# Kernel optimization log

Measured on AMD Instinct MI355X. Metric: run time of the kernel, lower is better.

Reference implementation:

```python
import jax, jax.numpy as jnp
import numpy as np

R = 2.0            # distance exponent
Q = 1.0            # activation exponent
SPECIFICITY = 1.0  # c in exp(-c * dist)
BETA = 3.0         # lateral competition exponent
TEMP_COMP = 1.0    # ClusterCompetition temperature
TEMP_WTA = 0.1     # SoftWTA temperature
PHI = 1.5          # association scaling
NEG_INF = -1e30

B, C, D = 1024, 512, 256


def setup_inputs() -> dict:
    key = jax.random.key(0)
    k1, k2, k3, k4, k5 = jax.random.split(key, 5)
    inp = jax.random.normal(k1, (B, D), dtype=jnp.float32)
    w_dist = jax.random.normal(k2, (C, D), dtype=jnp.float32)      # cluster centers
    attn = jax.random.uniform(k3, (D,), dtype=jnp.float32)         # dim-wise attention (>=0)
    w_assoc = jax.random.normal(k4, (C, 2), dtype=jnp.float32)     # association weights
    mask = jax.random.randint(k5, (C,), 0, 2, dtype=jnp.int32)     # recruited-cluster mask
    return {"inp": inp, "w_dist": w_dist, "attn": attn, "w_assoc": w_assoc, "mask": mask}


def reference(inp, w_dist, attn, w_assoc, mask):
    m = mask.astype(inp.dtype)                       # [C] 0/1 recruited gate
    # Distance: per-dim |x - w|^r for every (item, cluster) pair -> [B, C, D]
    dim_dist = jnp.abs(inp[:, None, :] - w_dist[None, :, :]) ** R
    # DimWiseAttention: sum-to-one constrained attention over dims
    a = attn / jnp.sum(attn)
    # ClusterActivation: H_j = exp(-c * (sum_d a_d * dist_d)^(q/r)) -> [B, C]
    wdist = jnp.einsum('bcd,d->bc', dim_dist, a)
    H = jnp.exp(-SPECIFICITY * wdist ** (Q / R))
    clusters_actv = H * m                            # MaskNonRecruit
    nonzero = m > 0
    # ClusterCompetition: softmax over recruited clusters of actv^beta (temp-scaled),
    # re-weighting each cluster's own activation.
    comp_logits = jnp.where(nonzero, BETA * jnp.log(H) / TEMP_COMP, NEG_INF)
    p_comp = jax.nn.softmax(comp_logits, axis=-1)
    competed = p_comp * clusters_actv                # [B, C]
    # SoftWTA: plain temperature softmax over recruited clusters, same re-weighting.
    wta_logits = jnp.where(nonzero, competed / TEMP_WTA, NEG_INF)
    p_wta = jax.nn.softmax(wta_logits, axis=-1)
    softwta = p_wta * competed                       # [B, C]
    # Classification: Phi-scaled linear readout to 2 classes.
    y_pred = PHI * (softwta @ w_assoc)               # [B, 2]
    return y_pred
```

## Files before the change

### kernel.cpp

```cpp
#include <hip/hip_runtime.h>
#include <math.h>

#define BN 1024
#define CN 512
#define DN 256
#define ROWS 4
#define DW 32

#define XS_OFF 0
#define WT_OFF (BN * DN)

#define NEG_INF_F (-1e30f)

__device__ __forceinline__ float waveMax(float v) {
    #pragma unroll
    for (int off = 32; off > 0; off >>= 1) v = fmaxf(v, __shfl_xor(v, off));
    return v;
}
__device__ __forceinline__ float waveSum(float v) {
    #pragma unroll
    for (int off = 32; off > 0; off >>= 1) v += __shfl_xor(v, off);
    return v;
}

__launch_bounds__(256, 4)
__global__ void prep_kernel(const float* __restrict__ inp, const float* __restrict__ wd,
                            const float* __restrict__ attn, float* __restrict__ ws) {
    __shared__ float red4[4];
    __shared__ float sarr[DN];
    __shared__ __align__(16) float tile[64][65];

    const int tid  = threadIdx.x;
    const int lane = tid & 63;

    float av = attn[tid];
    float s = av;
    #pragma unroll
    for (int off = 32; off > 0; off >>= 1) s += __shfl_xor(s, off);
    if (lane == 0) red4[tid >> 6] = s;
    __syncthreads();
    const float sv = sqrtf(av / (red4[0] + red4[1] + red4[2] + red4[3]));
    sarr[tid] = sv;
    __syncthreads();

    const int blk = blockIdx.x;
    if (blk < BN / 4) {
        #pragma unroll
        for (int i = 0; i < 4; ++i) {
            const int r = blk * 4 + i;
            ws[XS_OFF + r * DN + tid] = inp[r * DN + tid] * sv;
        }
    } else {
        const int tb = blk - BN / 4;
        const int c0 = (tb & 7) * 64;
        const int d0 = (tb >> 3) * 64;
        const int cr = tid >> 2;
        const int q  = tid & 3;
        #pragma unroll
        for (int i = 0; i < 4; ++i) {
            const int dd = q * 16 + i * 4;
            float4 w4 = *(const float4*)&wd[(c0 + cr) * DN + d0 + dd];
            w4.x *= sarr[d0 + dd + 0]; w4.y *= sarr[d0 + dd + 1];
            w4.z *= sarr[d0 + dd + 2]; w4.w *= sarr[d0 + dd + 3];
            *(float4*)&tile[cr][dd] = w4;
        }
        __syncthreads();
        const int dr = tid >> 2;
        #pragma unroll
        for (int i = 0; i < 4; ++i) {
            const int cc = q * 16 + i * 4;
            float4 o = {tile[cc + 0][dr], tile[cc + 1][dr],
                        tile[cc + 2][dr], tile[cc + 3][dr]};
            *(float4*)&ws[WT_OFF + (d0 + dr) * CN + c0 + cc] = o;
        }
    }
}

__launch_bounds__(512, 1)
__global__ void dist_kernel(const float* __restrict__ ws, const int* __restrict__ mask,
                            const float* __restrict__ w_assoc, float* __restrict__ y) {
    __shared__ float comb[8 * 32 * 64];

    const int tid  = threadIdx.x;
    const int lane = tid & 63;
    const int wz   = __builtin_amdgcn_readfirstlane(tid >> 6);
    const int b0   = blockIdx.x * ROWS;

    const float* xs = ws + XS_OFF;
    const float* wT = ws + WT_OFF;
    const int d0w = wz * DW;

    float acc[ROWS][8] = {};

    #pragma unroll
    for (int ch = 0; ch < DW / 4; ++ch) {
        const int d0 = d0w + ch * 4;
        float4 xv[ROWS];
        #pragma unroll
        for (int rr = 0; rr < ROWS; ++rr) {
            const int idx = __builtin_amdgcn_readfirstlane((b0 + rr) * DN + d0);
            xv[rr] = *(const float4*)&xs[idx];
        }
        #pragma unroll
        for (int dd = 0; dd < 4; ++dd) {
            const float* wrow = &wT[(size_t)(d0 + dd) * CN];
            const float4 wa = *(const float4*)&wrow[4 * lane];
            const float4 wb = *(const float4*)&wrow[256 + 4 * lane];
            #pragma unroll
            for (int rr = 0; rr < ROWS; ++rr) {
                const float xu = (dd == 0) ? xv[rr].x : (dd == 1) ? xv[rr].y
                               : (dd == 2) ? xv[rr].z : xv[rr].w;
                float e;
                e = xu - wa.x; acc[rr][0] = fmaf(e, e, acc[rr][0]);
                e = xu - wa.y; acc[rr][1] = fmaf(e, e, acc[rr][1]);
                e = xu - wa.z; acc[rr][2] = fmaf(e, e, acc[rr][2]);
                e = xu - wa.w; acc[rr][3] = fmaf(e, e, acc[rr][3]);
                e = xu - wb.x; acc[rr][4] = fmaf(e, e, acc[rr][4]);
                e = xu - wb.y; acc[rr][5] = fmaf(e, e, acc[rr][5]);
                e = xu - wb.z; acc[rr][6] = fmaf(e, e, acc[rr][6]);
                e = xu - wb.w; acc[rr][7] = fmaf(e, e, acc[rr][7]);
            }
        }
    }

    #pragma unroll
    for (int rr = 0; rr < ROWS; ++rr)
        #pragma unroll
        for (int j = 0; j < 8; ++j)
            comb[(wz * 32 + rr * 8 + j) * 64 + lane] = acc[rr][j];
    __syncthreads();

    if (wz < ROWS) {
        const int rr = wz;
        float dist[8] = {};
        #pragma unroll
        for (int zz = 0; zz < 8; ++zz)
            #pragma unroll
            for (int j = 0; j < 8; ++j)
                dist[j] += comb[(zz * 32 + rr * 8 + j) * 64 + lane];

        float t[8]; bool rec[8];
        const int4 m0 = *(const int4*)&mask[4 * lane];
        const int4 m1 = *(const int4*)&mask[256 + 4 * lane];
        rec[0] = m0.x > 0; rec[1] = m0.y > 0; rec[2] = m0.z > 0; rec[3] = m0.w > 0;
        rec[4] = m1.x > 0; rec[5] = m1.y > 0; rec[6] = m1.z > 0; rec[7] = m1.w > 0;
        #pragma unroll
        for (int j = 0; j < 8; ++j) t[j] = sqrtf(dist[j]);

        float l1[8], lmax = NEG_INF_F;
        #pragma unroll
        for (int j = 0; j < 8; ++j) { l1[j] = rec[j] ? (-3.0f * t[j]) : NEG_INF_F; lmax = fmaxf(lmax, l1[j]); }
        const float mx1 = waveMax(lmax);
        float e1[8], lsum = 0.f;
        #pragma unroll
        for (int j = 0; j < 8; ++j) { e1[j] = rec[j] ? expf(l1[j] - mx1) : 0.f; lsum += e1[j]; }
        const float inv_s1 = 1.0f / waveSum(lsum);

        float competed[8];
        #pragma unroll
        for (int j = 0; j < 8; ++j) competed[j] = e1[j] * inv_s1 * expf(-t[j]);

        float l2[8]; lmax = NEG_INF_F;
        #pragma unroll
        for (int j = 0; j < 8; ++j) { l2[j] = rec[j] ? (competed[j] * 10.0f) : NEG_INF_F; lmax = fmaxf(lmax, l2[j]); }
        const float mx2 = waveMax(lmax);
        float e2[8]; lsum = 0.f;
        #pragma unroll
        for (int j = 0; j < 8; ++j) { e2[j] = rec[j] ? expf(l2[j] - mx2) : 0.f; lsum += e2[j]; }
        const float inv_s2 = 1.0f / waveSum(lsum);

        const float4 waA = *(const float4*)&w_assoc[8 * lane];
        const float4 waB = *(const float4*)&w_assoc[8 * lane + 4];
        const float4 waC = *(const float4*)&w_assoc[512 + 8 * lane];
        const float4 waD = *(const float4*)&w_assoc[512 + 8 * lane + 4];
        float sw[8];
        #pragma unroll
        for (int j = 0; j < 8; ++j) sw[j] = e2[j] * inv_s2 * competed[j];
        float y0 = 0.f, y1 = 0.f;
        y0 = fmaf(sw[0], waA.x, y0); y1 = fmaf(sw[0], waA.y, y1);
        y0 = fmaf(sw[1], waA.z, y0); y1 = fmaf(sw[1], waA.w, y1);
        y0 = fmaf(sw[2], waB.x, y0); y1 = fmaf(sw[2], waB.y, y1);
        y0 = fmaf(sw[3], waB.z, y0); y1 = fmaf(sw[3], waB.w, y1);
        y0 = fmaf(sw[4], waC.x, y0); y1 = fmaf(sw[4], waC.y, y1);
        y0 = fmaf(sw[5], waC.z, y0); y1 = fmaf(sw[5], waC.w, y1);
        y0 = fmaf(sw[6], waD.x, y0); y1 = fmaf(sw[6], waD.y, y1);
        y0 = fmaf(sw[7], waD.z, y0); y1 = fmaf(sw[7], waD.w, y1);
        y0 = waveSum(y0);
        y1 = waveSum(y1);
        if (lane == 0) {
            float2 o = {1.5f * y0, 1.5f * y1};
            *(float2*)&y[(b0 + rr) * 2] = o;
        }
    }
}

extern "C" void kernel_launch(void* const* d_in, const int* in_sizes, int n_in,
                              void* d_out, int out_size, void* d_ws, size_t ws_size,
                              hipStream_t stream) {
    const float* inp     = (const float*)d_in[0];
    const float* w_dist  = (const float*)d_in[1];
    const float* attn    = (const float*)d_in[2];
    const float* w_assoc = (const float*)d_in[3];
    const int*   mask    = (const int*)d_in[4];
    float* out = (float*)d_out;
    float* ws  = (float*)d_ws;

    prep_kernel<<<BN / 4 + 32, 256, 0, stream>>>(inp, w_dist, attn, ws);
    dist_kernel<<<BN / ROWS, 512, 0, stream>>>(ws, mask, w_assoc, out);
}
```

Baseline: 74.70 us.

## Expand squared distance into norms minus dot product

Rewrites the weighted squared distance as ||x||_a^2 + ||w||_a^2 - 2<a*x, w>. The prep kernel now computes per-row and per-cluster weighted norms and scales only the inputs by the attention weights. The inner loop of the main kernel then does one FMA per element instead of a subtract plus an FMA. In exchange the prep kernel launches more blocks, and the expansion can lose precision through cancellation, which the code clamps at zero.

```diff
diff --git a/kernel.cpp b/kernel.cpp
--- a/kernel.cpp
+++ b/kernel.cpp
@@ -8,7 +8,9 @@
 #define DW 32
 
 #define XS_OFF 0
-#define WT_OFF (BN * DN)
+#define R_OFF  (BN * DN)
+#define Q_OFF  (R_OFF + BN)
+#define WT_OFF (Q_OFF + CN)
 
 #define NEG_INF_F (-1e30f)
 
@@ -27,11 +29,11 @@
 __global__ void prep_kernel(const float* __restrict__ inp, const float* __restrict__ wd,
                             const float* __restrict__ attn, float* __restrict__ ws) {
     __shared__ float red4[4];
-    __shared__ float sarr[DN];
     __shared__ __align__(16) float tile[64][65];
 
     const int tid  = threadIdx.x;
     const int lane = tid & 63;
+    const int blk  = blockIdx.x;
 
     float av = attn[tid];
     float s = av;
@@ -39,36 +41,42 @@
     for (int off = 32; off > 0; off >>= 1) s += __shfl_xor(s, off);
     if (lane == 0) red4[tid >> 6] = s;
     __syncthreads();
-    const float sv = sqrtf(av / (red4[0] + red4[1] + red4[2] + red4[3]));
-    sarr[tid] = sv;
+    const float a = av / (red4[0] + red4[1] + red4[2] + red4[3]);
     __syncthreads();
 
-    const int blk = blockIdx.x;
-    if (blk < BN / 4) {
-        #pragma unroll
-        for (int i = 0; i < 4; ++i) {
-            const int r = blk * 4 + i;
-            ws[XS_OFF + r * DN + tid] = inp[r * DN + tid] * sv;
-        }
+    if (blk < BN) {
+        const float x = inp[blk * DN + tid];
+        ws[XS_OFF + blk * DN + tid] = a * x;
+        float c = a * x * x;
+        #pragma unroll
+        for (int off = 32; off > 0; off >>= 1) c += __shfl_xor(c, off);
+        if (lane == 0) red4[tid >> 6] = c;
+        __syncthreads();
+        if (tid == 0) ws[R_OFF + blk] = red4[0] + red4[1] + red4[2] + red4[3];
+    } else if (blk < BN + CN) {
+        const float w = wd[(blk - BN) * DN + tid];
+        float c = a * w * w;
+        #pragma unroll
+        for (int off = 32; off > 0; off >>= 1) c += __shfl_xor(c, off);
+        if (lane == 0) red4[tid >> 6] = c;
+        __syncthreads();
+        if (tid == 0) ws[Q_OFF + (blk - BN)] = red4[0] + red4[1] + red4[2] + red4[3];
     } else {
-        const int tb = blk - BN / 4;
+        const int tb = blk - (BN + CN);
         const int c0 = (tb & 7) * 64;
         const int d0 = (tb >> 3) * 64;
         const int cr = tid >> 2;
-        const int q  = tid & 3;
+        const int qq = tid & 3;
         #pragma unroll
         for (int i = 0; i < 4; ++i) {
-            const int dd = q * 16 + i * 4;
-            float4 w4 = *(const float4*)&wd[(c0 + cr) * DN + d0 + dd];
-            w4.x *= sarr[d0 + dd + 0]; w4.y *= sarr[d0 + dd + 1];
-            w4.z *= sarr[d0 + dd + 2]; w4.w *= sarr[d0 + dd + 3];
-            *(float4*)&tile[cr][dd] = w4;
+            const int dd = qq * 16 + i * 4;
+            *(float4*)&tile[cr][dd] = *(const float4*)&wd[(c0 + cr) * DN + d0 + dd];
         }
         __syncthreads();
         const int dr = tid >> 2;
         #pragma unroll
         for (int i = 0; i < 4; ++i) {
-            const int cc = q * 16 + i * 4;
+            const int cc = qq * 16 + i * 4;
             float4 o = {tile[cc + 0][dr], tile[cc + 1][dr],
                         tile[cc + 2][dr], tile[cc + 3][dr]};
             *(float4*)&ws[WT_OFF + (d0 + dr) * CN + c0 + cc] = o;
@@ -90,7 +98,7 @@
     const float* wT = ws + WT_OFF;
     const int d0w = wz * DW;
 
-    float acc[ROWS][8] = {};
+    float dot[ROWS][8] = {};
 
     #pragma unroll
     for (int ch = 0; ch < DW / 4; ++ch) {
@@ -110,15 +118,14 @@
             for (int rr = 0; rr < ROWS; ++rr) {
                 const float xu = (dd == 0) ? xv[rr].x : (dd == 1) ? xv[rr].y
                                : (dd == 2) ? xv[rr].z : xv[rr].w;
-                float e;
-                e = xu - wa.x; acc[rr][0] = fmaf(e, e, acc[rr][0]);
-                e = xu - wa.y; acc[rr][1] = fmaf(e, e, acc[rr][1]);
-                e = xu - wa.z; acc[rr][2] = fmaf(e, e, acc[rr][2]);
-                e = xu - wa.w; acc[rr][3] = fmaf(e, e, acc[rr][3]);
-                e = xu - wb.x; acc[rr][4] = fmaf(e, e, acc[rr][4]);
-                e = xu - wb.y; acc[rr][5] = fmaf(e, e, acc[rr][5]);
-                e = xu - wb.z; acc[rr][6] = fmaf(e, e, acc[rr][6]);
-                e = xu - wb.w; acc[rr][7] = fmaf(e, e, acc[rr][7]);
+                dot[rr][0] = fmaf(xu, wa.x, dot[rr][0]);
+                dot[rr][1] = fmaf(xu, wa.y, dot[rr][1]);
+                dot[rr][2] = fmaf(xu, wa.z, dot[rr][2]);
+                dot[rr][3] = fmaf(xu, wa.w, dot[rr][3]);
+                dot[rr][4] = fmaf(xu, wb.x, dot[rr][4]);
+                dot[rr][5] = fmaf(xu, wb.y, dot[rr][5]);
+                dot[rr][6] = fmaf(xu, wb.z, dot[rr][6]);
+                dot[rr][7] = fmaf(xu, wb.w, dot[rr][7]);
             }
         }
     }
@@ -127,17 +134,22 @@
     for (int rr = 0; rr < ROWS; ++rr)
         #pragma unroll
         for (int j = 0; j < 8; ++j)
-            comb[(wz * 32 + rr * 8 + j) * 64 + lane] = acc[rr][j];
+            comb[(wz * 32 + rr * 8 + j) * 64 + lane] = dot[rr][j];
     __syncthreads();
 
     if (wz < ROWS) {
         const int rr = wz;
-        float dist[8] = {};
+        float dsum[8] = {};
         #pragma unroll
         for (int zz = 0; zz < 8; ++zz)
             #pragma unroll
             for (int j = 0; j < 8; ++j)
-                dist[j] += comb[(zz * 32 + rr * 8 + j) * 64 + lane];
+                dsum[j] += comb[(zz * 32 + rr * 8 + j) * 64 + lane];
+
+        const float rb = ws[R_OFF + b0 + rr];
+        const float4 q0 = *(const float4*)&ws[Q_OFF + 4 * lane];
+        const float4 q1 = *(const float4*)&ws[Q_OFF + 256 + 4 * lane];
+        const float qv[8] = {q0.x, q0.y, q0.z, q0.w, q1.x, q1.y, q1.z, q1.w};
 
         float t[8]; bool rec[8];
         const int4 m0 = *(const int4*)&mask[4 * lane];
@@ -145,7 +157,8 @@
         rec[0] = m0.x > 0; rec[1] = m0.y > 0; rec[2] = m0.z > 0; rec[3] = m0.w > 0;
         rec[4] = m1.x > 0; rec[5] = m1.y > 0; rec[6] = m1.z > 0; rec[7] = m1.w > 0;
         #pragma unroll
-        for (int j = 0; j < 8; ++j) t[j] = sqrtf(dist[j]);
+        for (int j = 0; j < 8; ++j)
+            t[j] = sqrtf(fmaxf(rb + qv[j] - 2.0f * dsum[j], 0.0f));
 
         float l1[8], lmax = NEG_INF_F;
         #pragma unroll
@@ -205,6 +218,6 @@
     float* out = (float*)d_out;
     float* ws  = (float*)d_ws;
 
-    prep_kernel<<<BN / 4 + 32, 256, 0, stream>>>(inp, w_dist, attn, ws);
+    prep_kernel<<<BN + CN + 32, 256, 0, stream>>>(inp, w_dist, attn, ws);
     dist_kernel<<<BN / ROWS, 512, 0, stream>>>(ws, mask, w_assoc, out);
 }
```

Result: no change. 74.14 us (-0.8%).
